# Kernel optimization log

Hardware: AMD Instinct MI355X
Metric: run time of the kernel (lower is better)

## Reference

```python
import jax, jax.numpy as jnp
import numpy as np

NEG_SLOPE = 0.2
BN_EPS = 1e-5


def _gat(x, src, dst, W, a_src, a_dst, b, concat):
    """PyG GATConv (eval mode, self-loops already in src/dst)."""
    N = x.shape[0]
    H, C = a_src.shape
    h = (x @ W).reshape(N, H, C)                      # [N,H,C]
    s = (h * a_src).sum(-1)                           # [N,H] per-node src score
    d = (h * a_dst).sum(-1)                           # [N,H] per-node dst score
    e = jax.nn.leaky_relu(s[src] + d[dst], NEG_SLOPE)  # [E,H]
    m = jax.ops.segment_max(e, dst, num_segments=N)   # segment softmax over dst
    ex = jnp.exp(e - m[dst])
    denom = jax.ops.segment_sum(ex, dst, num_segments=N)
    alpha = ex / denom[dst]                           # [E,H]
    out = jax.ops.segment_sum(alpha[:, :, None] * h[src], dst, num_segments=N)  # [N,H,C]
    out = out.reshape(N, H * C) if concat else out.mean(axis=1)
    return out + b


def _bn(x, g, beta, rm, rv):
    return (x - rm) * (g / jnp.sqrt(rv + BN_EPS)) + beta


def setup_inputs() -> dict:
    key = jax.random.key(0)
    ks = jax.random.split(key, 32)
    N, E, IN, HID, H, NC = 50000, 400000, 768, 128, 4, 2
    d = {}
    d['x'] = jax.random.normal(ks[0], (N, IN), jnp.float32)
    d['edge_index'] = jax.random.randint(ks[1], (2, E), 0, N, jnp.int64)

    def lin(k, fan_in, shape):
        return jax.random.normal(k, shape, jnp.float32) * (1.0 / np.sqrt(fan_in))

    # layer 1: in=768 -> 4 heads x 128, concat
    d['W1'] = lin(ks[2], IN, (IN, H * HID)); d['a1s'] = lin(ks[3], HID, (H, HID))
    d['a1d'] = lin(ks[4], HID, (H, HID)); d['b1'] = jnp.zeros((H * HID,), jnp.float32)
    d['g1'] = jax.random.uniform(ks[5], (H * HID,), jnp.float32, 0.5, 1.5)
    d['be1'] = jax.random.normal(ks[6], (H * HID,), jnp.float32) * 0.1
    d['rm1'] = jax.random.normal(ks[7], (H * HID,), jnp.float32) * 0.1
    d['rv1'] = jax.random.uniform(ks[8], (H * HID,), jnp.float32, 0.5, 1.5)
    d['W2'] = lin(ks[9], H * HID, (H * HID, H * HID)); d['a2s'] = lin(ks[10], HID, (H, HID))
    d['a2d'] = lin(ks[11], HID, (H, HID)); d['b2'] = jnp.zeros((H * HID,), jnp.float32)
    d['g2'] = jax.random.uniform(ks[12], (H * HID,), jnp.float32, 0.5, 1.5)
    d['be2'] = jax.random.normal(ks[13], (H * HID,), jnp.float32) * 0.1
    d['rm2'] = jax.random.normal(ks[14], (H * HID,), jnp.float32) * 0.1
    d['rv2'] = jax.random.uniform(ks[15], (H * HID,), jnp.float32, 0.5, 1.5)
    # layer 3: 512 -> 1 head x 128, mean (concat=False)
    d['W3'] = lin(ks[16], H * HID, (H * HID, HID)); d['a3s'] = lin(ks[17], HID, (1, HID))
    d['a3d'] = lin(ks[18], HID, (1, HID)); d['b3'] = jnp.zeros((HID,), jnp.float32)
    d['g3'] = jax.random.uniform(ks[19], (HID,), jnp.float32, 0.5, 1.5)
    d['be3'] = jax.random.normal(ks[20], (HID,), jnp.float32) * 0.1
    d['rm3'] = jax.random.normal(ks[21], (HID,), jnp.float32) * 0.1
    d['rv3'] = jax.random.uniform(ks[22], (HID,), jnp.float32, 0.5, 1.5)
    # classifier 128 -> 2
    d['Wc'] = lin(ks[23], HID, (HID, NC)); d['bc'] = jnp.zeros((NC,), jnp.float32)
    return d


def reference(x, edge_index, W1, a1s, a1d, b1, g1, be1, rm1, rv1,
              W2, a2s, a2d, b2, g2, be2, rm2, rv2,
              W3, a3s, a3d, b3, g3, be3, rm3, rv3, Wc, bc):
    N = x.shape[0]
    loops = jnp.arange(N, dtype=edge_index.dtype)  # GATConv add_self_loops=True
    src = jnp.concatenate([edge_index[0], loops])
    dst = jnp.concatenate([edge_index[1], loops])

    h = _gat(x, src, dst, W1, a1s, a1d, b1, concat=True)
    h = jax.nn.elu(_bn(h, g1, be1, rm1, rv1))          # dropout: eval mode (identity)
    h = _gat(h, src, dst, W2, a2s, a2d, b2, concat=True)
    h = jax.nn.elu(_bn(h, g2, be2, rm2, rv2))
    h = _gat(h, src, dst, W3, a3s, a3d, b3, concat=False)
    h = jax.nn.elu(_bn(h, g3, be3, rm3, rv3))
    return h @ Wc + bc                                  # [N, 2] logits
```

## Files before the change

### kernel.cpp

```cpp
#include <hip/hip_runtime.h>
#include <hip/hip_bf16.h>
#include <math.h>

constexpr int IN_F = 768;
constexpr float NEG_SLOPE = 0.2f;
constexpr float BN_EPS = 1e-5f;

typedef __attribute__((ext_vector_type(8))) short short8;
typedef __attribute__((ext_vector_type(4))) float f32x4;

__device__ inline float bf2f(unsigned short u) {
    unsigned int x = ((unsigned int)u) << 16;
    return __uint_as_float(x);
}
__device__ inline unsigned short f2bf(float f) {
    __hip_bfloat16 h = __float2bfloat16(f);
    return *(unsigned short*)&h;
}
__device__ inline void gload_lds16(const unsigned short* g, unsigned short* l) {
    __builtin_amdgcn_global_load_lds(
        (const __attribute__((address_space(1))) void*)g,
        (__attribute__((address_space(3))) void*)l, 16, 0, 0);
}


__global__ void init_counts(int* __restrict__ count, int* __restrict__ cursor, int N) {
    int i = blockIdx.x * blockDim.x + threadIdx.x;
    if (i < N) { count[i] = 1; cursor[i] = 0; }
}

__global__ void count_edges(const int* __restrict__ dst, int E, int* __restrict__ count) {
    int e = blockIdx.x * blockDim.x + threadIdx.x;
    if (e < E) atomicAdd(&count[dst[e]], 1);
}

__global__ void scan_counts(const int* __restrict__ count, int* __restrict__ row_start, int N) {
    __shared__ int wsum[17];
    __shared__ int carry;
    int tid = threadIdx.x;
    int lane = tid & 63, w = tid >> 6;
    if (tid == 0) carry = 0;
    __syncthreads();
    for (int base = 0; base < N; base += 4096) {
        int idx = base + tid * 4;
        int v0 = (idx + 0 < N) ? count[idx + 0] : 0;
        int v1 = (idx + 1 < N) ? count[idx + 1] : 0;
        int v2 = (idx + 2 < N) ? count[idx + 2] : 0;
        int v3 = (idx + 3 < N) ? count[idx + 3] : 0;
        int tsum = v0 + v1 + v2 + v3;
        int x = tsum;
        #pragma unroll
        for (int off = 1; off < 64; off <<= 1) {
            int y = __shfl_up(x, off, 64);
            if (lane >= off) x += y;
        }
        if (lane == 63) wsum[w] = x;
        __syncthreads();
        if (tid == 0) {
            int r = 0;
            for (int i = 0; i < 16; i++) { int t = wsum[i]; wsum[i] = r; r += t; }
            wsum[16] = r;
        }
        __syncthreads();
        int excl = carry + wsum[w] + (x - tsum);
        if (idx + 0 < N) row_start[idx + 0] = excl;
        if (idx + 1 < N) row_start[idx + 1] = excl + v0;
        if (idx + 2 < N) row_start[idx + 2] = excl + v0 + v1;
        if (idx + 3 < N) row_start[idx + 3] = excl + v0 + v1 + v2;
        __syncthreads();
        if (tid == 0) carry += wsum[16];
        __syncthreads();
    }
    if (tid == 0) row_start[N] = carry;
}

__global__ void scatter_edges(const int* __restrict__ srcA, const int* __restrict__ dstA,
                              int E, int N, const int* __restrict__ row_start,
                              int* __restrict__ cursor, int* __restrict__ col,
                              int* __restrict__ dstn) {
    int i = blockIdx.x * blockDim.x + threadIdx.x;
    if (i < E) {
        int d = dstA[i];
        int pos = row_start[d] + atomicAdd(&cursor[d], 1);
        col[pos] = srcA[i];
        dstn[pos] = d;
    } else if (i < E + N) {
        int n = i - E;
        int pos = row_start[n] + atomicAdd(&cursor[n], 1);
        col[pos] = n;
        dstn[pos] = n;
    }
}


__global__ void cast_x_bf16(const float* __restrict__ x, unsigned short* __restrict__ xb,
                            long total) {
    long i = ((long)blockIdx.x * blockDim.x + threadIdx.x) * 4;
    if (i >= total) return;
    float4 v = *(const float4*)&x[i];
    *(ushort2*)&xb[i] = make_ushort2(f2bf(v.x), f2bf(v.y));
    *(ushort2*)&xb[i + 2] = make_ushort2(f2bf(v.z), f2bf(v.w));
}

__global__ void cast_transpose_w(const float* __restrict__ W, unsigned short* __restrict__ Wt,
                                 int K, int Ncols) {
    int idx = blockIdx.x * blockDim.x + threadIdx.x;
    if (idx >= K * Ncols) return;
    int k = idx / Ncols, n = idx % Ncols;
    Wt[(size_t)n * K + k] = f2bf(W[idx]);
}


__global__ __launch_bounds__(256) void gemm_bf16(const unsigned short* __restrict__ A,
                                                 const unsigned short* __restrict__ Wt,
                                                 unsigned short* __restrict__ C,
                                                 const float* __restrict__ a_s,
                                                 const float* __restrict__ a_d,
                                                 float* __restrict__ s2, float* __restrict__ d2,
                                                 int M, int Nc, int K, int H) {
    __shared__ __align__(16) unsigned short As[128 * 32];
    __shared__ __align__(16) unsigned short Bs[128 * 32];
    const int tid = threadIdx.x;
    const int lane = tid & 63;
    const int wave = tid >> 6;
    const int wm = wave >> 1, wn = wave & 1;
    const int by = blockIdx.x;
    const int row0 = blockIdx.y * 128, col0 = by * 128;

    f32x4 acc[4][4];
    #pragma unroll
    for (int i = 0; i < 4; i++)
        #pragma unroll
        for (int j = 0; j < 4; j++)
            acc[i][j] = (f32x4){0.f, 0.f, 0.f, 0.f};

    const int ldm = tid >> 2;
    const int kpart = (tid & 3) * 8;
    const int khalf = (lane >> 4) * 8;
    const int fr = lane & 15;
    const int quad = lane >> 4;

    for (int k0 = 0; k0 < K; k0 += 32) {
        __syncthreads();
        #pragma unroll
        for (int i = 0; i < 2; i++) {
            int gr = row0 + i * 64 + ldm; if (gr >= M) gr = M - 1;
            gload_lds16(A + (size_t)gr * K + k0 + kpart, &As[i * 2048 + tid * 8]);
            int n = col0 + i * 64 + ldm;
            gload_lds16(Wt + (size_t)n * K + k0 + kpart, &Bs[i * 2048 + tid * 8]);
        }
        __syncthreads();
        short8 a[4], b[4];
        #pragma unroll
        for (int t = 0; t < 4; t++) {
            a[t] = *(const short8*)&As[(wm * 64 + t * 16 + fr) * 32 + khalf];
            b[t] = *(const short8*)&Bs[(wn * 64 + t * 16 + fr) * 32 + khalf];
        }
        #pragma unroll
        for (int mi = 0; mi < 4; mi++)
            #pragma unroll
            for (int ni = 0; ni < 4; ni++)
                acc[mi][ni] = __builtin_amdgcn_mfma_f32_16x16x32_bf16(
                    a[mi], b[ni], acc[mi][ni], 0, 0, 0);
    }

    const int rbase = row0 + wm * 64 + quad * 4;
    const int cbase = col0 + wn * 64 + fr;
    #pragma unroll
    for (int mi = 0; mi < 4; mi++) {
        #pragma unroll
        for (int reg = 0; reg < 4; reg++) {
            int r = rbase + mi * 16 + reg;
            if (r < M) {
                #pragma unroll
                for (int ni = 0; ni < 4; ni++)
                    C[(size_t)r * Nc + cbase + ni * 16] = f2bf(acc[mi][ni][reg]);
            }
        }
    }

    float asv[4], adv[4];
    #pragma unroll
    for (int ni = 0; ni < 4; ni++) {
        int c = by * 128 + wn * 64 + ni * 16 + fr;
        asv[ni] = a_s[c];
        adv[ni] = a_d[c];
    }
    float ps[4][4], pd[4][4];
    #pragma unroll
    for (int mi = 0; mi < 4; mi++)
        #pragma unroll
        for (int reg = 0; reg < 4; reg++) {
            float t = 0.f, u = 0.f;
            #pragma unroll
            for (int ni = 0; ni < 4; ni++) {
                t += acc[mi][ni][reg] * asv[ni];
                u += acc[mi][ni][reg] * adv[ni];
            }
            ps[mi][reg] = t;
            pd[mi][reg] = u;
        }
    #pragma unroll
    for (int off = 1; off <= 8; off <<= 1)
        #pragma unroll
        for (int mi = 0; mi < 4; mi++)
            #pragma unroll
            for (int reg = 0; reg < 4; reg++) {
                ps[mi][reg] += __shfl_xor(ps[mi][reg], off, 64);
                pd[mi][reg] += __shfl_xor(pd[mi][reg], off, 64);
            }
    float oS = 0.f, oD = 0.f;
    #pragma unroll
    for (int mi = 0; mi < 4; mi++)
        #pragma unroll
        for (int reg = 0; reg < 4; reg++)
            if (fr == mi * 4 + reg) { oS = ps[mi][reg]; oD = pd[mi][reg]; }
    int rw = rbase + (fr >> 2) * 16 + (fr & 3);
    if (rw < M) {
        s2[(size_t)rw * (2 * H) + wn * H + by] = oS;
        d2[(size_t)rw * (2 * H) + wn * H + by] = oD;
    }
}


template <int H>
__global__ void edge_weights(const int* __restrict__ col, const int* __restrict__ dstn,
                             const float* __restrict__ s2, const float* __restrict__ d2,
                             float* __restrict__ wgt, int P) {
    int p = blockIdx.x * blockDim.x + threadIdx.x;
    if (p >= P) return;
    int sn = col[p], dn = dstn[p];
    if (H == 4) {
        float4 sa = *(const float4*)&s2[sn * 8];
        float4 sb = *(const float4*)&s2[sn * 8 + 4];
        float4 da = *(const float4*)&d2[dn * 8];
        float4 db = *(const float4*)&d2[dn * 8 + 4];
        float4 o;
        float e;
        e = sa.x + sb.x + da.x + db.x; e = e > 0.f ? e : NEG_SLOPE * e; o.x = __expf(e);
        e = sa.y + sb.y + da.y + db.y; e = e > 0.f ? e : NEG_SLOPE * e; o.y = __expf(e);
        e = sa.z + sb.z + da.z + db.z; e = e > 0.f ? e : NEG_SLOPE * e; o.z = __expf(e);
        e = sa.w + sb.w + da.w + db.w; e = e > 0.f ? e : NEG_SLOPE * e; o.w = __expf(e);
        *(float4*)&wgt[p * 4] = o;
    } else {
        float e = s2[sn * 2] + s2[sn * 2 + 1] + d2[dn * 2] + d2[dn * 2 + 1];
        e = e > 0.f ? e : NEG_SLOPE * e;
        wgt[p] = __expf(e);
    }
}


__global__ void gat_agg_h4(const unsigned short* __restrict__ h, const float* __restrict__ wgt,
                           const int* __restrict__ row_start, const int* __restrict__ col,
                           const float* __restrict__ bias,
                           const float* __restrict__ gam, const float* __restrict__ beta,
                           const float* __restrict__ rm, const float* __restrict__ rv,
                           unsigned short* __restrict__ out, int N) {
    int lane = threadIdx.x & 63;
    int wv = threadIdx.x >> 6;
    int n = blockIdx.x * 4 + wv;
    if (n >= N) return;
    int beg = row_start[n], end = row_start[n + 1];
    int hh = lane >> 4;
    int ch0 = lane * 8;

    float acc[8] = {0.f, 0.f, 0.f, 0.f, 0.f, 0.f, 0.f, 0.f};
    float denom = 0.f;

    for (int i = beg; i < end; i += 8) {
        uint4 raw[8]; float w[8];
        #pragma unroll
        for (int u = 0; u < 8; u++) {
            int e0 = i + u;
            int e = e0 < end ? e0 : end - 1;
            int sn = col[e];
            w[u] = (e0 < end) ? wgt[e * 4 + hh] : 0.f;
            raw[u] = *(const uint4*)&h[(size_t)sn * 512 + ch0];
        }
        #pragma unroll
        for (int u = 0; u < 8; u++) {
            denom += w[u];
            acc[0] += w[u] * bf2f((unsigned short)(raw[u].x & 0xffff));
            acc[1] += w[u] * bf2f((unsigned short)(raw[u].x >> 16));
            acc[2] += w[u] * bf2f((unsigned short)(raw[u].y & 0xffff));
            acc[3] += w[u] * bf2f((unsigned short)(raw[u].y >> 16));
            acc[4] += w[u] * bf2f((unsigned short)(raw[u].z & 0xffff));
            acc[5] += w[u] * bf2f((unsigned short)(raw[u].z >> 16));
            acc[6] += w[u] * bf2f((unsigned short)(raw[u].w & 0xffff));
            acc[7] += w[u] * bf2f((unsigned short)(raw[u].w >> 16));
        }
    }
    float inv = 1.f / denom;
    float v[8];
    #pragma unroll
    for (int c = 0; c < 8; c++) {
        int ch = ch0 + c;
        float t = acc[c] * inv + bias[ch];
        t = (t - rm[ch]) * (gam[ch] * rsqrtf(rv[ch] + BN_EPS)) + beta[ch];
        v[c] = t > 0.f ? t : expf(t) - 1.f;
    }
    uint4 p;
    p.x = (unsigned int)f2bf(v[0]) | ((unsigned int)f2bf(v[1]) << 16);
    p.y = (unsigned int)f2bf(v[2]) | ((unsigned int)f2bf(v[3]) << 16);
    p.z = (unsigned int)f2bf(v[4]) | ((unsigned int)f2bf(v[5]) << 16);
    p.w = (unsigned int)f2bf(v[6]) | ((unsigned int)f2bf(v[7]) << 16);
    *(uint4*)&out[(size_t)n * 512 + ch0] = p;
}


__global__ void gat_agg_h1_cls(const unsigned short* __restrict__ h, const float* __restrict__ wgt,
                               const int* __restrict__ row_start, const int* __restrict__ col,
                               const float* __restrict__ bias,
                               const float* __restrict__ gam, const float* __restrict__ beta,
                               const float* __restrict__ rm, const float* __restrict__ rv,
                               const float* __restrict__ Wc, const float* __restrict__ bc,
                               float* __restrict__ out, int N) {
    int lane = threadIdx.x & 63;
    int wv = threadIdx.x >> 6;
    int n = blockIdx.x * 4 + wv;
    if (n >= N) return;
    int beg = row_start[n], end = row_start[n + 1];
    int q = lane >> 4;
    int fl = lane & 15;
    const size_t hoff = fl * 8;

    float acc[8] = {0.f, 0.f, 0.f, 0.f, 0.f, 0.f, 0.f, 0.f};
    float denom = 0.f;

    for (int i = beg; i < end; i += 16) {
        uint4 raw[4]; float w[4];
        #pragma unroll
        for (int u = 0; u < 4; u++) {
            int e0 = i + u * 4 + q;
            int e = e0 < end ? e0 : end - 1;
            int sn = col[e];
            w[u] = (e0 < end) ? wgt[e] : 0.f;
            raw[u] = *(const uint4*)&h[(size_t)sn * 128 + hoff];
        }
        #pragma unroll
        for (int u = 0; u < 4; u++) {
            denom += w[u];
            acc[0] += w[u] * bf2f((unsigned short)(raw[u].x & 0xffff));
            acc[1] += w[u] * bf2f((unsigned short)(raw[u].x >> 16));
            acc[2] += w[u] * bf2f((unsigned short)(raw[u].y & 0xffff));
            acc[3] += w[u] * bf2f((unsigned short)(raw[u].y >> 16));
            acc[4] += w[u] * bf2f((unsigned short)(raw[u].z & 0xffff));
            acc[5] += w[u] * bf2f((unsigned short)(raw[u].z >> 16));
            acc[6] += w[u] * bf2f((unsigned short)(raw[u].w & 0xffff));
            acc[7] += w[u] * bf2f((unsigned short)(raw[u].w >> 16));
        }
    }
    #pragma unroll
    for (int c = 0; c < 8; c++) {
        acc[c] += __shfl_xor(acc[c], 16, 64);
        acc[c] += __shfl_xor(acc[c], 32, 64);
    }
    denom += __shfl_xor(denom, 16, 64);
    denom += __shfl_xor(denom, 32, 64);

    if (q == 0) {
        float inv = 1.f / denom;
        int ch0 = fl * 8;
        float p0 = 0.f, p1 = 0.f;
        #pragma unroll
        for (int c = 0; c < 8; c++) {
            int ch = ch0 + c;
            float t = acc[c] * inv + bias[ch];
            t = (t - rm[ch]) * (gam[ch] * rsqrtf(rv[ch] + BN_EPS)) + beta[ch];
            t = t > 0.f ? t : expf(t) - 1.f;
            p0 += t * Wc[ch * 2 + 0];
            p1 += t * Wc[ch * 2 + 1];
        }
        #pragma unroll
        for (int off = 8; off >= 1; off >>= 1) {
            p0 += __shfl_xor(p0, off, 64);
            p1 += __shfl_xor(p1, off, 64);
        }
        if (fl == 0) {
            out[n * 2 + 0] = p0 + bc[0];
            out[n * 2 + 1] = p1 + bc[1];
        }
    }
}


extern "C" void kernel_launch(void* const* d_in, const int* in_sizes, int n_in,
                              void* d_out, int out_size, void* d_ws, size_t ws_size,
                              hipStream_t stream) {
    const float* x   = (const float*)d_in[0];
    const int*   ei  = (const int*)d_in[1];
    const float* W1  = (const float*)d_in[2];
    const float* a1s = (const float*)d_in[3];
    const float* a1d = (const float*)d_in[4];
    const float* b1  = (const float*)d_in[5];
    const float* gm1 = (const float*)d_in[6];
    const float* be1 = (const float*)d_in[7];
    const float* rm1 = (const float*)d_in[8];
    const float* rv1 = (const float*)d_in[9];
    const float* W2  = (const float*)d_in[10];
    const float* a2s = (const float*)d_in[11];
    const float* a2d = (const float*)d_in[12];
    const float* b2  = (const float*)d_in[13];
    const float* gm2 = (const float*)d_in[14];
    const float* be2 = (const float*)d_in[15];
    const float* rm2 = (const float*)d_in[16];
    const float* rv2 = (const float*)d_in[17];
    const float* W3  = (const float*)d_in[18];
    const float* a3s = (const float*)d_in[19];
    const float* a3d = (const float*)d_in[20];
    const float* b3  = (const float*)d_in[21];
    const float* gm3 = (const float*)d_in[22];
    const float* be3 = (const float*)d_in[23];
    const float* rm3 = (const float*)d_in[24];
    const float* rv3 = (const float*)d_in[25];
    const float* Wc  = (const float*)d_in[26];
    const float* bc  = (const float*)d_in[27];

    int N = in_sizes[0] / IN_F;
    int E = in_sizes[1] / 2;
    int P = E + N;
    const int* srcA = ei;
    const int* dstA = ei + E;

    unsigned short* xb   = (unsigned short*)d_ws;
    unsigned short* hbuf = xb + (size_t)N * 768;
    unsigned short* gbuf = hbuf + (size_t)N * 512;
    float* s2   = (float*)(gbuf + (size_t)N * 512);
    float* d2   = s2 + (size_t)N * 8;
    float* wgt  = d2 + (size_t)N * 8;
    unsigned short* Wt1 = (unsigned short*)(wgt + (size_t)P * 4);
    unsigned short* Wt2 = Wt1 + 512 * 768;
    unsigned short* Wt3 = Wt2 + 512 * 512;
    int* count     = (int*)(Wt3 + 128 * 512);
    int* cursor    = count + N;
    int* row_start = cursor + N;
    int* col       = row_start + N + 1;
    int* dstn      = col + P;

    init_counts<<<(N + 255) / 256, 256, 0, stream>>>(count, cursor, N);
    count_edges<<<(E + 255) / 256, 256, 0, stream>>>(dstA, E, count);
    scan_counts<<<1, 1024, 0, stream>>>(count, row_start, N);
    scatter_edges<<<(E + N + 255) / 256, 256, 0, stream>>>(srcA, dstA, E, N, row_start,
                                                           cursor, col, dstn);
    long xtot = (long)N * IN_F;
    cast_x_bf16<<<(int)((xtot / 4 + 255) / 256), 256, 0, stream>>>(x, xb, xtot);
    cast_transpose_w<<<(768 * 512 + 255) / 256, 256, 0, stream>>>(W1, Wt1, 768, 512);
    cast_transpose_w<<<(512 * 512 + 255) / 256, 256, 0, stream>>>(W2, Wt2, 512, 512);
    cast_transpose_w<<<(512 * 128 + 255) / 256, 256, 0, stream>>>(W3, Wt3, 512, 128);

    int Mb = (N + 127) / 128;
    int Nb4 = (N + 3) / 4;

    gemm_bf16<<<dim3(4, Mb), 256, 0, stream>>>(xb, Wt1, hbuf, a1s, a1d, s2, d2, N, 512, 768, 4);
    edge_weights<4><<<(P + 255) / 256, 256, 0, stream>>>(col, dstn, s2, d2, wgt, P);
    gat_agg_h4<<<Nb4, 256, 0, stream>>>(hbuf, wgt, row_start, col,
                                        b1, gm1, be1, rm1, rv1, gbuf, N);
    gemm_bf16<<<dim3(4, Mb), 256, 0, stream>>>(gbuf, Wt2, hbuf, a2s, a2d, s2, d2, N, 512, 512, 4);
    edge_weights<4><<<(P + 255) / 256, 256, 0, stream>>>(col, dstn, s2, d2, wgt, P);
    gat_agg_h4<<<Nb4, 256, 0, stream>>>(hbuf, wgt, row_start, col,
                                        b2, gm2, be2, rm2, rv2, gbuf, N);
    gemm_bf16<<<dim3(1, Mb), 256, 0, stream>>>(gbuf, Wt3, hbuf, a3s, a3d, s2, d2, N, 128, 512, 1);
    edge_weights<1><<<(P + 255) / 256, 256, 0, stream>>>(col, dstn, s2, d2, wgt, P);
    gat_agg_h1_cls<<<Nb4, 256, 0, stream>>>(hbuf, wgt, row_start, col,
                                            b3, gm3, be3, rm3, rv3, Wc, bc, (float*)d_out, N);
}
```

Before: 733.3 us.

## Swizzle GEMM LDS layout, remap block order, fuse weight casts, set occupancy hint

The three weight cast/transpose kernels are merged into one launch. The GEMM block index is remapped into groups of 8 row tiles so that neighbouring blocks share A rows across column tiles, which should improve L2 reuse. An XOR swizzle on the k-chunk in the LDS writes and reads is meant to cut LDS bank conflicts on the fragment loads. A launch_bounds minimum of 3 blocks per CU is added, which may constrain register allocation.

```diff
diff --git a/kernel.cpp b/kernel.cpp
--- a/kernel.cpp
+++ b/kernel.cpp
@@ -102,30 +102,50 @@
     *(ushort2*)&xb[i + 2] = make_ushort2(f2bf(v.z), f2bf(v.w));
 }
 
-__global__ void cast_transpose_w(const float* __restrict__ W, unsigned short* __restrict__ Wt,
-                                 int K, int Ncols) {
+__global__ void cast_w_all(const float* __restrict__ W1, const float* __restrict__ W2,
+                           const float* __restrict__ W3, unsigned short* __restrict__ Wt1,
+                           unsigned short* __restrict__ Wt2, unsigned short* __restrict__ Wt3) {
     int idx = blockIdx.x * blockDim.x + threadIdx.x;
-    if (idx >= K * Ncols) return;
-    int k = idx / Ncols, n = idx % Ncols;
-    Wt[(size_t)n * K + k] = f2bf(W[idx]);
-}
-
-
-__global__ __launch_bounds__(256) void gemm_bf16(const unsigned short* __restrict__ A,
-                                                 const unsigned short* __restrict__ Wt,
-                                                 unsigned short* __restrict__ C,
-                                                 const float* __restrict__ a_s,
-                                                 const float* __restrict__ a_d,
-                                                 float* __restrict__ s2, float* __restrict__ d2,
-                                                 int M, int Nc, int K, int H) {
+    const int S1 = 768 * 512, S2 = 512 * 512, S3 = 512 * 128;
+    if (idx < S1) {
+        int k = idx / 512, n = idx % 512;
+        Wt1[(size_t)n * 768 + k] = f2bf(W1[idx]);
+    } else if (idx < S1 + S2) {
+        int j = idx - S1;
+        int k = j / 512, n = j % 512;
+        Wt2[(size_t)n * 512 + k] = f2bf(W2[j]);
+    } else if (idx < S1 + S2 + S3) {
+        int j = idx - S1 - S2;
+        int k = j / 128, n = j % 128;
+        Wt3[(size_t)n * 512 + k] = f2bf(W3[j]);
+    }
+}
+
+
+__global__ __launch_bounds__(256, 3) void gemm_bf16(const unsigned short* __restrict__ A,
+                                                    const unsigned short* __restrict__ Wt,
+                                                    unsigned short* __restrict__ C,
+                                                    const float* __restrict__ a_s,
+                                                    const float* __restrict__ a_d,
+                                                    float* __restrict__ s2,
+                                                    float* __restrict__ d2,
+                                                    int M, int Nc, int K, int H) {
     __shared__ __align__(16) unsigned short As[128 * 32];
     __shared__ __align__(16) unsigned short Bs[128 * 32];
     const int tid = threadIdx.x;
     const int lane = tid & 63;
     const int wave = tid >> 6;
     const int wm = wave >> 1, wn = wave & 1;
-    const int by = blockIdx.x;
-    const int row0 = blockIdx.y * 128, col0 = by * 128;
+
+    const int l = blockIdx.x;
+    const int x = l & 7;
+    const int t0 = l >> 3;
+    const int HT = Nc >> 7;
+    const int by = (HT == 4) ? (t0 & 3) : 0;
+    const int g  = (HT == 4) ? (t0 >> 2) : t0;
+    const int rb = g * 8 + x;
+    const int row0 = rb * 128, col0 = by * 128;
+    if (row0 >= M) return;
 
     f32x4 acc[4][4];
     #pragma unroll
@@ -135,10 +155,10 @@
             acc[i][j] = (f32x4){0.f, 0.f, 0.f, 0.f};
 
     const int ldm = tid >> 2;
-    const int kpart = (tid & 3) * 8;
-    const int khalf = (lane >> 4) * 8;
+    const int kpart = (((tid & 3) ^ ((tid >> 2) & 3)) * 8);
     const int fr = lane & 15;
     const int quad = lane >> 4;
+    const int kchunk8 = ((quad ^ (fr & 3)) * 8);
 
     for (int k0 = 0; k0 < K; k0 += 32) {
         __syncthreads();
@@ -152,9 +172,9 @@
         __syncthreads();
         short8 a[4], b[4];
         #pragma unroll
-        for (int t = 0; t < 4; t++) {
-            a[t] = *(const short8*)&As[(wm * 64 + t * 16 + fr) * 32 + khalf];
-            b[t] = *(const short8*)&Bs[(wn * 64 + t * 16 + fr) * 32 + khalf];
+        for (int tt = 0; tt < 4; tt++) {
+            a[tt] = *(const short8*)&As[(wm * 64 + tt * 16 + fr) * 32 + kchunk8];
+            b[tt] = *(const short8*)&Bs[(wn * 64 + tt * 16 + fr) * 32 + kchunk8];
         }
         #pragma unroll
         for (int mi = 0; mi < 4; mi++)
@@ -444,22 +464,22 @@
                                                            cursor, col, dstn);
     long xtot = (long)N * IN_F;
     cast_x_bf16<<<(int)((xtot / 4 + 255) / 256), 256, 0, stream>>>(x, xb, xtot);
-    cast_transpose_w<<<(768 * 512 + 255) / 256, 256, 0, stream>>>(W1, Wt1, 768, 512);
-    cast_transpose_w<<<(512 * 512 + 255) / 256, 256, 0, stream>>>(W2, Wt2, 512, 512);
-    cast_transpose_w<<<(512 * 128 + 255) / 256, 256, 0, stream>>>(W3, Wt3, 512, 128);
+    cast_w_all<<<(768 * 512 + 512 * 512 + 512 * 128 + 255) / 256, 256, 0, stream>>>(
+        W1, W2, W3, Wt1, Wt2, Wt3);
 
     int Mb = (N + 127) / 128;
+    int MbP = (Mb + 7) & ~7;
     int Nb4 = (N + 3) / 4;
 
-    gemm_bf16<<<dim3(4, Mb), 256, 0, stream>>>(xb, Wt1, hbuf, a1s, a1d, s2, d2, N, 512, 768, 4);
+    gemm_bf16<<<4 * MbP, 256, 0, stream>>>(xb, Wt1, hbuf, a1s, a1d, s2, d2, N, 512, 768, 4);
     edge_weights<4><<<(P + 255) / 256, 256, 0, stream>>>(col, dstn, s2, d2, wgt, P);
     gat_agg_h4<<<Nb4, 256, 0, stream>>>(hbuf, wgt, row_start, col,
                                         b1, gm1, be1, rm1, rv1, gbuf, N);
-    gemm_bf16<<<dim3(4, Mb), 256, 0, stream>>>(gbuf, Wt2, hbuf, a2s, a2d, s2, d2, N, 512, 512, 4);
+    gemm_bf16<<<4 * MbP, 256, 0, stream>>>(gbuf, Wt2, hbuf, a2s, a2d, s2, d2, N, 512, 512, 4);
     edge_weights<4><<<(P + 255) / 256, 256, 0, stream>>>(col, dstn, s2, d2, wgt, P);
     gat_agg_h4<<<Nb4, 256, 0, stream>>>(hbuf, wgt, row_start, col,
                                         b2, gm2, be2, rm2, rv2, gbuf, N);
-    gemm_bf16<<<dim3(1, Mb), 256, 0, stream>>>(gbuf, Wt3, hbuf, a3s, a3d, s2, d2, N, 128, 512, 1);
+    gemm_bf16<<<MbP, 256, 0, stream>>>(gbuf, Wt3, hbuf, a3s, a3d, s2, d2, N, 128, 512, 1);
     edge_weights<1><<<(P + 255) / 256, 256, 0, stream>>>(col, dstn, s2, d2, wgt, P);
     gat_agg_h1_cls<<<Nb4, 256, 0, stream>>>(hbuf, wgt, row_start, col,
                                             b3, gm3, be3, rm3, rv3, Wc, bc, (float*)d_out, N);
```

Result: faster. 690.9 us (-5.8%).
